# Optimization experiments

Measured on AMD Instinct MI355X. Metric: run time of the kernel, lower is better.

Reference implementation:

```python
import jax, jax.numpy as jnp
import numpy as np

V0 = 32000  # medicine vocab; SOS = V0, END = V0 + 1
E = 1024    # emb_dim


def setup_inputs() -> dict:
    key = jax.random.key(0)
    ks = jax.random.split(key, 12)
    s = 0.02
    return {
        "input_diagnosis": jax.random.randint(ks[0], (128,), 0, 35501),
        "input_procedure": jax.random.randint(ks[1], (64,), 0, 35501),
        "input_medicine": jax.random.randint(ks[2], (128,), 0, 35501),
        "dec_tokens": jax.random.randint(ks[3], (64,), 0, V0),
        "enc_emb": jax.random.normal(ks[4], (35501, E), jnp.float32) * s,
        "dec_emb": jax.random.normal(ks[5], (V0 + 2, E), jnp.float32) * s,
        "attn_w": jax.random.normal(ks[6], (1, 2 * E), jnp.float32) * s,
        "attn_b": jnp.zeros((1,), jnp.float32),
        "gru_w_ih": jax.random.normal(ks[7], (3 * E, 2 * E), jnp.float32) * s,
        "gru_w_hh": jax.random.normal(ks[8], (3 * E, E), jnp.float32) * s,
        "gru_b_ih": jnp.zeros((3 * E,), jnp.float32),
        "gru_b_hh": jnp.zeros((3 * E,), jnp.float32),
        "out_w": jax.random.normal(ks[9], (V0 + 2, E), jnp.float32) * s,
        "out_b": jnp.zeros((V0 + 2,), jnp.float32),
    }


def reference(input_diagnosis, input_procedure, input_medicine, dec_tokens,
              enc_emb, dec_emb, attn_w, attn_b,
              gru_w_ih, gru_w_hh, gru_b_ih, gru_b_hh, out_w, out_b):
    # Context: concat of the three code-set embeddings -> [L, E]
    ctx = jnp.concatenate([enc_emb[input_diagnosis],
                           enc_emb[input_procedure],
                           enc_emb[input_medicine]], axis=0)
    # Teacher-forced decoder token sequence: [SOS] + targets -> [T]
    tokens = jnp.concatenate([jnp.array([V0], dec_tokens.dtype), dec_tokens])
    dec_x = dec_emb[tokens]  # [T, E]
    h0 = dec_x[0]            # hidden init = SOS embedding (hidden_state None branch)
    # Additive attention Linear(2E,1): split weight into hidden part / context part
    w_h = attn_w[0, :E]
    w_e = attn_w[0, E:]
    ctx_score = ctx @ w_e + attn_b[0]  # [L], precomputed once

    def step(h, x):
        scores = ctx_score + jnp.dot(h, w_h)          # [L]
        a = jax.nn.softmax(scores)
        c = a @ ctx                                    # [E] weighted context
        u = jnp.concatenate([c, x])                    # [2E] GRU input
        gi = gru_w_ih @ u + gru_b_ih
        gh = gru_w_hh @ h + gru_b_hh
        ir, iz, in_ = jnp.split(gi, 3)
        hr, hz, hn = jnp.split(gh, 3)
        r = jax.nn.sigmoid(ir + hr)
        z = jax.nn.sigmoid(iz + hz)
        n = jnp.tanh(in_ + r * hn)
        h_new = (1.0 - z) * n + z * h                  # PyTorch GRU cell
        logits = out_w @ jax.nn.relu(h_new) + out_b    # [V0+2]
        return h_new, logits

    _, logits = jax.lax.scan(step, h0, dec_x)          # [T, V0+2]
    return logits
```

## Files before the change

kernel.cpp:

```cpp
#include <hip/hip_runtime.h>
#include <hip/hip_cooperative_groups.h>

typedef unsigned long long u64;
#define V0TOK 32000
#define EDIM  1024

__device__ __forceinline__ float dot4(float4 a, float4 b) {
    return fmaf(a.x, b.x, fmaf(a.y, b.y, fmaf(a.z, b.z, a.w * b.w)));
}

__global__ __launch_bounds__(512, 1) void k_rnn(
    const int* __restrict__ diag, const int* __restrict__ proc,
    const int* __restrict__ med,  const int* __restrict__ dtok,
    const float* __restrict__ enc, const float* __restrict__ dec,
    const float* __restrict__ attw,
    const float* __restrict__ wih, const float* __restrict__ whh,
    const float* __restrict__ bih, const float* __restrict__ bhh,
    float* __restrict__ ctx_ws, float* __restrict__ c_ws,
    unsigned* __restrict__ cnt, float* __restrict__ hbuf,
    float* __restrict__ hrelu)
{
    const int b = blockIdx.x, tid = threadIdx.x;
    const int w = tid >> 6, l = tid & 63;

    __shared__ float Wx[24 * 1024];
    __shared__ float sm[320];
    __shared__ float red1[8], red2[8];
    __shared__ float hlds[1024];

    if (tid == 0)
        __hip_atomic_store(&cnt[b * 16], 0u, __ATOMIC_RELAXED, __HIP_MEMORY_SCOPE_AGENT);
    if (b < 40) {
        int i = 8*b + w;
        int ridx = (i < 128) ? diag[i] : (i < 192 ? proc[i-128] : med[i-192]);
        const float4* row = (const float4*)(enc + (size_t)ridx * EDIM);
        const float4* we  = (const float4*)(attw + EDIM);
        float p = 0.f;
        #pragma unroll
        for (int m = 0; m < 4; m++) p += dot4(row[l + 64*m], we[l + 64*m]);
        #pragma unroll
        for (int off = 32; off; off >>= 1) p += __shfl_xor(p, off);
        if (l == 0) ctx_ws[i] = p;
    }
    __threadfence();
    cooperative_groups::this_grid().sync();
    __threadfence();

    {
        float s1 = (tid < 320) ? ctx_ws[tid] : -1e30f;
        float mx = s1;
        #pragma unroll
        for (int off = 32; off; off >>= 1) mx = fmaxf(mx, __shfl_xor(mx, off));
        if (l == 0) red1[w] = mx;
        __syncthreads();
        mx = red1[0];
        #pragma unroll
        for (int k = 1; k < 8; k++) mx = fmaxf(mx, red1[k]);
        float e1 = (tid < 320) ? expf(s1 - mx) : 0.f;
        float ss = e1;
        #pragma unroll
        for (int off = 32; off; off >>= 1) ss += __shfl_xor(ss, off);
        if (l == 0) red2[w] = ss;
        __syncthreads();
        float tot = red2[0];
        #pragma unroll
        for (int k = 1; k < 8; k++) tot += red2[k];
        if (tid < 320) sm[tid] = e1 / tot;
        __syncthreads();

        int e = 8*b + w;
        float p = 0.f;
        for (int i = l; i < 320; i += 64) {
            int ridx = (i < 128) ? diag[i] : (i < 192 ? proc[i-128] : med[i-192]);
            p += sm[i] * enc[(size_t)ridx * EDIM + e];
        }
        #pragma unroll
        for (int off = 32; off; off >>= 1) p += __shfl_xor(p, off);
        if (l == 0) c_ws[e] = p;
    }
    __threadfence();
    cooperative_groups::this_grid().sync();
    __threadfence();

    const int jr = 8*b + w, jz = 1024 + jr, jn = 2048 + jr;

    {
        const float4* s_r = (const float4*)(wih + (size_t)jr * 2048 + 1024);
        const float4* s_z = (const float4*)(wih + (size_t)jz * 2048 + 1024);
        const float4* s_n = (const float4*)(wih + (size_t)jn * 2048 + 1024);
        float4* d_r = (float4*)(Wx + (0*8 + w) * 1024);
        float4* d_z = (float4*)(Wx + (1*8 + w) * 1024);
        float4* d_n = (float4*)(Wx + (2*8 + w) * 1024);
        #pragma unroll
        for (int m = 0; m < 4; m++) {
            d_r[l + 64*m] = s_r[l + 64*m];
            d_z[l + 64*m] = s_z[l + 64*m];
            d_n[l + 64*m] = s_n[l + 64*m];
        }
    }

    float4 whr[4], whz[4], whn[4];
    {
        const float4* qr = (const float4*)(whh + (size_t)jr * 1024);
        const float4* qz = (const float4*)(whh + (size_t)jz * 1024);
        const float4* qn = (const float4*)(whh + (size_t)jn * 1024);
        #pragma unroll
        for (int m = 0; m < 4; m++) { whr[m] = qr[l + 64*m]; whz[m] = qz[l + 64*m]; whn[m] = qn[l + 64*m]; }
    }

    float4 c4[4], h4[4];
    {
        const float4* cp = (const float4*)c_ws;
        const float4* hp = (const float4*)(dec + (size_t)V0TOK * EDIM);
        #pragma unroll
        for (int m = 0; m < 4; m++) { c4[m] = cp[l + 64*m]; h4[m] = hp[l + 64*m]; }
    }
    const float b_r  = bih[jr] + bhh[jr];
    const float b_z  = bih[jz] + bhh[jz];
    const float b_ni = bih[jn];
    const float b_nh = bhh[jn];

    float gic_r = 0.f, gic_z = 0.f, gic_n = 0.f;
    {
        const float4* pr = (const float4*)(wih + (size_t)jr * 2048);
        const float4* pz = (const float4*)(wih + (size_t)jz * 2048);
        const float4* pn = (const float4*)(wih + (size_t)jn * 2048);
        #pragma unroll
        for (int m = 0; m < 4; m++) {
            gic_r += dot4(pr[l + 64*m], c4[m]);
            gic_z += dot4(pz[l + 64*m], c4[m]);
            gic_n += dot4(pn[l + 64*m], c4[m]);
        }
    }

    __syncthreads();

    const float4* WxR = (const float4*)(Wx + (0*8 + w) * 1024);
    const float4* WxZ = (const float4*)(Wx + (1*8 + w) * 1024);
    const float4* WxN = (const float4*)(Wx + (2*8 + w) * 1024);

    int tokreg = dtok[l];

    float gxr = gic_r, gxz = gic_z, gxn = gic_n;
    #pragma unroll
    for (int m = 0; m < 4; m++) {
        gxr += dot4(WxR[l + 64*m], h4[m]);
        gxz += dot4(WxZ[l + 64*m], h4[m]);
        gxn += dot4(WxN[l + 64*m], h4[m]);
    }
    float4 xv[4];
    {
        int tok1 = __shfl(tokreg, 0);
        const float4* xp = (const float4*)(dec + (size_t)tok1 * EDIM);
        #pragma unroll
        for (int m = 0; m < 4; m++) xv[m] = xp[l + 64*m];
    }

    const int jmi = jr >> 8, jli = (jr & 255) >> 2, jci = jr & 3;

    for (int t = 0; t < 65; t++) {
        float hr = 0.f, hz = 0.f, hn_ = 0.f;
        #pragma unroll
        for (int m = 0; m < 4; m++) {
            hr  += dot4(whr[m], h4[m]);
            hz  += dot4(whz[m], h4[m]);
            hn_ += dot4(whn[m], h4[m]);
        }
        float sr = gxr + hr, sz = gxz + hz, sni = gxn, snh = hn_;
        #pragma unroll
        for (int off = 32; off; off >>= 1) {
            sr  += __shfl_xor(sr, off);  sz  += __shfl_xor(sz, off);
            sni += __shfl_xor(sni, off); snh += __shfl_xor(snh, off);
        }
        float rg = 1.f / (1.f + expf(-(sr + b_r)));
        float zg = 1.f / (1.f + expf(-(sz + b_z)));
        float ng = tanhf(sni + b_ni + rg * (snh + b_nh));

        float4 hs = (jmi == 0) ? h4[0] : (jmi == 1) ? h4[1] : (jmi == 2) ? h4[2] : h4[3];
        float hv0 = (jci == 0) ? hs.x : (jci == 1) ? hs.y : (jci == 2) ? hs.z : hs.w;
        float hv = __shfl(hv0, jli);
        float hnew = (1.f - zg) * ng + zg * hv;

        if (t < 64) {
            const int par = (t + 1) & 1;
            if (l == 0) {
                hrelu[t * 1024 + jr] = fmaxf(hnew, 0.f);
                __hip_atomic_store(&hbuf[par * 1024 + jr], hnew,
                                   __ATOMIC_RELAXED, __HIP_MEMORY_SCOPE_AGENT);
            }
            __syncthreads();
            if (tid == 0)
                __hip_atomic_fetch_add(&cnt[b * 16], 1u,
                                       __ATOMIC_RELAXED, __HIP_MEMORY_SCOPE_AGENT);

            gxr = gic_r; gxz = gic_z; gxn = gic_n;
            #pragma unroll
            for (int m = 0; m < 4; m++) {
                gxr += dot4(WxR[l + 64*m], xv[m]);
                gxz += dot4(WxZ[l + 64*m], xv[m]);
                gxn += dot4(WxN[l + 64*m], xv[m]);
            }
            if (t < 63) {
                int tok = __shfl(tokreg, t + 1);
                const float4* xp = (const float4*)(dec + (size_t)tok * EDIM);
                #pragma unroll
                for (int m = 0; m < 4; m++) xv[m] = xp[l + 64*m];
            }

            if (tid < 128) {
                const unsigned target = (unsigned)(t + 1);
                while (__hip_atomic_load(&cnt[tid * 16], __ATOMIC_RELAXED,
                                         __HIP_MEMORY_SCOPE_AGENT) < target)
                    __builtin_amdgcn_s_sleep(1);
            }
            __syncthreads();

            u64 v = __hip_atomic_load((u64*)hbuf + par * 512 + tid,
                                      __ATOMIC_RELAXED, __HIP_MEMORY_SCOPE_AGENT);
            ((u64*)hlds)[tid] = v;
            __syncthreads();
            #pragma unroll
            for (int m = 0; m < 4; m++) h4[m] = ((const float4*)hlds)[l + 64*m];
        } else {
            if (l == 0) hrelu[64 * 1024 + jr] = fmaxf(hnew, 0.f);
        }
    }
}

__global__ __launch_bounds__(512) void k_logits(
    const float* __restrict__ wo, const float* __restrict__ bo,
    const float* __restrict__ hrelu, float* __restrict__ out)
{
    __shared__ float Hs[65 * 68];
    const int tid = threadIdx.x;
    const int q = tid & 15, s = (tid >> 4) & 7, g = tid >> 7;
    const int v0 = blockIdx.x * 32;
    const int vb = v0 + 8 * g;

    const float* wbase = wo + (size_t)((vb < 32002) ? vb : 0) * 1024;

    float acc[8][9];
    #pragma unroll
    for (int r = 0; r < 8; r++)
        #pragma unroll
        for (int ti = 0; ti < 9; ti++) acc[r][ti] = 0.f;

    for (int kc = 0; kc < 16; kc++) {
        __syncthreads();
        for (int idx = tid; idx < 65 * 16; idx += 512) {
            int t = idx >> 4, m = idx & 15;
            *(float4*)(Hs + t * 68 + 4 * m) =
                *(const float4*)(hrelu + t * 1024 + kc * 64 + 4 * m);
        }
        float4 wv[8];
        #pragma unroll
        for (int r = 0; r < 8; r++) {
            int v = vb + r;
            const float* wr = (v < 32002) ? (wbase + (size_t)r * 1024) : wbase;
            wv[r] = *(const float4*)(wr + kc * 64 + 4 * q);
        }
        __syncthreads();

        #pragma unroll
        for (int ti = 0; ti < 9; ti++) {
            int t = s + 8 * ti;
            if (t < 65) {
                float4 h4 = *(const float4*)(Hs + t * 68 + 4 * q);
                #pragma unroll
                for (int r = 0; r < 8; r++) {
                    acc[r][ti] = fmaf(wv[r].x, h4.x, acc[r][ti]);
                    acc[r][ti] = fmaf(wv[r].y, h4.y, acc[r][ti]);
                    acc[r][ti] = fmaf(wv[r].z, h4.z, acc[r][ti]);
                    acc[r][ti] = fmaf(wv[r].w, h4.w, acc[r][ti]);
                }
            }
        }
    }

    __syncthreads();
    float* Os = Hs;
    #pragma unroll
    for (int ti = 0; ti < 9; ti++) {
        int t = s + 8 * ti;
        #pragma unroll
        for (int r = 0; r < 8; r++) {
            float sum = acc[r][ti];
            sum += __shfl_xor(sum, 1);
            sum += __shfl_xor(sum, 2);
            sum += __shfl_xor(sum, 4);
            sum += __shfl_xor(sum, 8);
            if (q == 0 && t < 65) Os[t * 33 + 8 * g + r] = sum;
        }
    }
    __syncthreads();
    for (int idx = tid; idx < 65 * 32; idx += 512) {
        int t = idx >> 5, c = idx & 31;
        int v = v0 + c;
        if (v < 32002) out[(size_t)t * 32002 + v] = Os[t * 33 + c] + bo[v];
    }
}

extern "C" void kernel_launch(void* const* d_in, const int* in_sizes, int n_in,
                              void* d_out, int out_size, void* d_ws, size_t ws_size,
                              hipStream_t stream) {
    const int*   diag = (const int*)d_in[0];
    const int*   proc = (const int*)d_in[1];
    const int*   med  = (const int*)d_in[2];
    const int*   dtok = (const int*)d_in[3];
    const float* enc  = (const float*)d_in[4];
    const float* dec  = (const float*)d_in[5];
    const float* attw = (const float*)d_in[6];
    const float* wih  = (const float*)d_in[8];
    const float* whh  = (const float*)d_in[9];
    const float* bih  = (const float*)d_in[10];
    const float* bhh  = (const float*)d_in[11];
    const float* wo   = (const float*)d_in[12];
    const float* bo   = (const float*)d_in[13];
    float* out = (float*)d_out;

    float*    ctx_ws = (float*)d_ws;
    float*    c_ws   = (float*)((char*)d_ws + 2048);
    unsigned* cnt    = (unsigned*)((char*)d_ws + 8192);
    float*    hbuf   = (float*)((char*)d_ws + 16384);
    float*    hrelu  = (float*)((char*)d_ws + 32768);

    void* args[] = { (void*)&diag, (void*)&proc, (void*)&med, (void*)&dtok,
                     (void*)&enc, (void*)&dec, (void*)&attw,
                     (void*)&wih, (void*)&whh, (void*)&bih, (void*)&bhh,
                     (void*)&ctx_ws, (void*)&c_ws, (void*)&cnt, (void*)&hbuf,
                     (void*)&hrelu };
    hipLaunchCooperativeKernel((void*)k_rnn, dim3(128), dim3(512), args, 0, stream);

    k_logits<<<dim3(1001), dim3(512), 0, stream>>>(wo, bo, hrelu, out);
}
```

Measured before the change: 512.7 us.

## Replace counter barrier with tagged hidden-state polling and retile logits GEMV

The recurrent kernel drops the per-block arrival counters and their syncthreads-plus-atomic barrier. Each block now writes its hidden values packed with a step tag into 64-bit slots, and readers spin until every slot carries the current tag. This removes a round trip through the counters and lets each element be consumed as soon as it arrives, but every thread now spins on global memory. Separately, the logits kernel is retiled to 16 vocab rows per 256-thread block with 65 accumulators per thread and a software-prefetched hrelu/weight stage, trading register pressure for lower LDS traffic and better occupancy.

```diff
diff --git a/kernel.cpp b/kernel.cpp
--- a/kernel.cpp
+++ b/kernel.cpp
@@ -17,8 +17,7 @@
     const float* __restrict__ wih, const float* __restrict__ whh,
     const float* __restrict__ bih, const float* __restrict__ bhh,
     float* __restrict__ ctx_ws, float* __restrict__ c_ws,
-    unsigned* __restrict__ cnt, float* __restrict__ hbuf,
-    float* __restrict__ hrelu)
+    u64* __restrict__ hbuf, float* __restrict__ hrelu)
 {
     const int b = blockIdx.x, tid = threadIdx.x;
     const int w = tid >> 6, l = tid & 63;
@@ -28,8 +27,9 @@
     __shared__ float red1[8], red2[8];
     __shared__ float hlds[1024];
 
-    if (tid == 0)
-        __hip_atomic_store(&cnt[b * 16], 0u, __ATOMIC_RELAXED, __HIP_MEMORY_SCOPE_AGENT);
+    if (b < 4)
+        __hip_atomic_store(&hbuf[b * 512 + tid], 0ull,
+                           __ATOMIC_RELAXED, __HIP_MEMORY_SCOPE_AGENT);
     if (b < 40) {
         int i = 8*b + w;
         int ridx = (i < 128) ? diag[i] : (i < 192 ? proc[i-128] : med[i-192]);
@@ -156,7 +156,7 @@
         for (int m = 0; m < 4; m++) xv[m] = xp[l + 64*m];
     }
 
-    const int jmi = jr >> 8, jli = (jr & 255) >> 2, jci = jr & 3;
+    const int jmi = jr >> 8, jli = (jr >> 2) & 63, jci = jr & 3;
 
     for (int t = 0; t < 65; t++) {
         float hr = 0.f, hz = 0.f, hn_ = 0.f;
@@ -183,15 +183,13 @@
 
         if (t < 64) {
             const int par = (t + 1) & 1;
+            const unsigned tag = (unsigned)(t + 1);
             if (l == 0) {
                 hrelu[t * 1024 + jr] = fmaxf(hnew, 0.f);
-                __hip_atomic_store(&hbuf[par * 1024 + jr], hnew,
+                u64 pk = ((u64)tag << 32) | (u64)__float_as_uint(hnew);
+                __hip_atomic_store(&hbuf[par * 1024 + jr], pk,
                                    __ATOMIC_RELAXED, __HIP_MEMORY_SCOPE_AGENT);
             }
-            __syncthreads();
-            if (tid == 0)
-                __hip_atomic_fetch_add(&cnt[b * 16], 1u,
-                                       __ATOMIC_RELAXED, __HIP_MEMORY_SCOPE_AGENT);
 
             gxr = gic_r; gxz = gic_z; gxn = gic_n;
             #pragma unroll
@@ -207,96 +205,98 @@
                 for (int m = 0; m < 4; m++) xv[m] = xp[l + 64*m];
             }
 
-            if (tid < 128) {
-                const unsigned target = (unsigned)(t + 1);
-                while (__hip_atomic_load(&cnt[tid * 16], __ATOMIC_RELAXED,
-                                         __HIP_MEMORY_SCOPE_AGENT) < target)
-                    __builtin_amdgcn_s_sleep(1);
+            {
+                u64* hb = hbuf + par * 1024;
+                u64 va, vb2;
+                while (1) {
+                    va  = __hip_atomic_load(&hb[2*tid],     __ATOMIC_RELAXED, __HIP_MEMORY_SCOPE_AGENT);
+                    vb2 = __hip_atomic_load(&hb[2*tid + 1], __ATOMIC_RELAXED, __HIP_MEMORY_SCOPE_AGENT);
+                    if (((unsigned)(va >> 32) == tag) & ((unsigned)(vb2 >> 32) == tag)) break;
+                }
+                hlds[2*tid]     = __uint_as_float((unsigned)va);
+                hlds[2*tid + 1] = __uint_as_float((unsigned)vb2);
             }
-            __syncthreads();
-
-            u64 v = __hip_atomic_load((u64*)hbuf + par * 512 + tid,
-                                      __ATOMIC_RELAXED, __HIP_MEMORY_SCOPE_AGENT);
-            ((u64*)hlds)[tid] = v;
             __syncthreads();
             #pragma unroll
             for (int m = 0; m < 4; m++) h4[m] = ((const float4*)hlds)[l + 64*m];
+            __syncthreads();
         } else {
             if (l == 0) hrelu[64 * 1024 + jr] = fmaxf(hnew, 0.f);
         }
     }
 }
 
-__global__ __launch_bounds__(512) void k_logits(
+__global__ __launch_bounds__(256, 4) void k_logits(
     const float* __restrict__ wo, const float* __restrict__ bo,
     const float* __restrict__ hrelu, float* __restrict__ out)
 {
     __shared__ float Hs[65 * 68];
-    const int tid = threadIdx.x;
-    const int q = tid & 15, s = (tid >> 4) & 7, g = tid >> 7;
-    const int v0 = blockIdx.x * 32;
-    const int vb = v0 + 8 * g;
-
-    const float* wbase = wo + (size_t)((vb < 32002) ? vb : 0) * 1024;
-
-    float acc[8][9];
+    const int tid = threadIdx.x, q = tid & 15, vl = tid >> 4;
+    const int v0 = blockIdx.x * 16;
+    const int v  = v0 + vl;
+    const int vc = (v < 32002) ? v : 32001;
+    const float* wrow = wo + (size_t)vc * 1024;
+
+    float acc[65];
     #pragma unroll
-    for (int r = 0; r < 8; r++)
-        #pragma unroll
-        for (int ti = 0; ti < 9; ti++) acc[r][ti] = 0.f;
+    for (int t = 0; t < 65; t++) acc[t] = 0.f;
+
+    float4 st0, st1, st2, st3, st4;
+    #define ISSUE(kc_) do {                                                   \
+        int base = (kc_) * 64;                                                \
+        { int idx = tid;       st0 = *(const float4*)(hrelu + (idx>>4)*1024 + base + 4*(idx&15)); } \
+        { int idx = tid + 256; st1 = *(const float4*)(hrelu + (idx>>4)*1024 + base + 4*(idx&15)); } \
+        { int idx = tid + 512; st2 = *(const float4*)(hrelu + (idx>>4)*1024 + base + 4*(idx&15)); } \
+        { int idx = tid + 768; st3 = *(const float4*)(hrelu + (idx>>4)*1024 + base + 4*(idx&15)); } \
+        if (tid < 16) st4 = *(const float4*)(hrelu + 64*1024 + base + 4*tid); \
+    } while (0)
+    #define WRITE() do {                                                      \
+        { int idx = tid;       *(float4*)(Hs + (idx>>4)*68 + 4*(idx&15)) = st0; } \
+        { int idx = tid + 256; *(float4*)(Hs + (idx>>4)*68 + 4*(idx&15)) = st1; } \
+        { int idx = tid + 512; *(float4*)(Hs + (idx>>4)*68 + 4*(idx&15)) = st2; } \
+        { int idx = tid + 768; *(float4*)(Hs + (idx>>4)*68 + 4*(idx&15)) = st3; } \
+        if (tid < 16) *(float4*)(Hs + 64*68 + 4*tid) = st4;                   \
+    } while (0)
+
+    ISSUE(0);
+    float4 wv = *(const float4*)(wrow + 4*q);
 
     for (int kc = 0; kc < 16; kc++) {
-        __syncthreads();
-        for (int idx = tid; idx < 65 * 16; idx += 512) {
-            int t = idx >> 4, m = idx & 15;
-            *(float4*)(Hs + t * 68 + 4 * m) =
-                *(const float4*)(hrelu + t * 1024 + kc * 64 + 4 * m);
-        }
-        float4 wv[8];
-        #pragma unroll
-        for (int r = 0; r < 8; r++) {
-            int v = vb + r;
-            const float* wr = (v < 32002) ? (wbase + (size_t)r * 1024) : wbase;
-            wv[r] = *(const float4*)(wr + kc * 64 + 4 * q);
-        }
-        __syncthreads();
-
-        #pragma unroll
-        for (int ti = 0; ti < 9; ti++) {
-            int t = s + 8 * ti;
-            if (t < 65) {
-                float4 h4 = *(const float4*)(Hs + t * 68 + 4 * q);
-                #pragma unroll
-                for (int r = 0; r < 8; r++) {
-                    acc[r][ti] = fmaf(wv[r].x, h4.x, acc[r][ti]);
-                    acc[r][ti] = fmaf(wv[r].y, h4.y, acc[r][ti]);
-                    acc[r][ti] = fmaf(wv[r].z, h4.z, acc[r][ti]);
-                    acc[r][ti] = fmaf(wv[r].w, h4.w, acc[r][ti]);
-                }
-            }
-        }
-    }
-
-    __syncthreads();
+        WRITE();
+        __syncthreads();
+        float4 wnext;
+        if (kc < 15) {
+            ISSUE(kc + 1);
+            wnext = *(const float4*)(wrow + (kc + 1) * 64 + 4*q);
+        }
+        const float* hp = Hs + 4*q;
+        #pragma unroll
+        for (int t = 0; t < 65; t++) {
+            float4 h4 = *(const float4*)(hp + t * 68);
+            acc[t] = fmaf(wv.x, h4.x, acc[t]);
+            acc[t] = fmaf(wv.y, h4.y, acc[t]);
+            acc[t] = fmaf(wv.z, h4.z, acc[t]);
+            acc[t] = fmaf(wv.w, h4.w, acc[t]);
+        }
+        wv = wnext;
+        __syncthreads();
+    }
+
     float* Os = Hs;
     #pragma unroll
-    for (int ti = 0; ti < 9; ti++) {
-        int t = s + 8 * ti;
-        #pragma unroll
-        for (int r = 0; r < 8; r++) {
-            float sum = acc[r][ti];
-            sum += __shfl_xor(sum, 1);
-            sum += __shfl_xor(sum, 2);
-            sum += __shfl_xor(sum, 4);
-            sum += __shfl_xor(sum, 8);
-            if (q == 0 && t < 65) Os[t * 33 + 8 * g + r] = sum;
-        }
+    for (int t = 0; t < 65; t++) {
+        float s_ = acc[t];
+        s_ += __shfl_xor(s_, 1);
+        s_ += __shfl_xor(s_, 2);
+        s_ += __shfl_xor(s_, 4);
+        s_ += __shfl_xor(s_, 8);
+        if (q == 0) Os[t * 17 + vl] = s_;
     }
     __syncthreads();
-    for (int idx = tid; idx < 65 * 32; idx += 512) {
-        int t = idx >> 5, c = idx & 31;
-        int v = v0 + c;
-        if (v < 32002) out[(size_t)t * 32002 + v] = Os[t * 33 + c] + bo[v];
+    for (int idx = tid; idx < 65 * 16; idx += 256) {
+        int t = idx >> 4, c = idx & 15;
+        int vv = v0 + c;
+        if (vv < 32002) out[(size_t)t * 32002 + vv] = Os[t * 17 + c] + bo[vv];
     }
 }
 
@@ -318,18 +318,16 @@
     const float* bo   = (const float*)d_in[13];
     float* out = (float*)d_out;
 
-    float*    ctx_ws = (float*)d_ws;
-    float*    c_ws   = (float*)((char*)d_ws + 2048);
-    unsigned* cnt    = (unsigned*)((char*)d_ws + 8192);
-    float*    hbuf   = (float*)((char*)d_ws + 16384);
-    float*    hrelu  = (float*)((char*)d_ws + 32768);
+    float* ctx_ws = (float*)d_ws;
+    float* c_ws   = (float*)((char*)d_ws + 2048);
+    u64*   hbuf   = (u64*)  ((char*)d_ws + 16384);
+    float* hrelu  = (float*)((char*)d_ws + 32768);
 
     void* args[] = { (void*)&diag, (void*)&proc, (void*)&med, (void*)&dtok,
                      (void*)&enc, (void*)&dec, (void*)&attw,
                      (void*)&wih, (void*)&whh, (void*)&bih, (void*)&bhh,
-                     (void*)&ctx_ws, (void*)&c_ws, (void*)&cnt, (void*)&hbuf,
-                     (void*)&hrelu };
+                     (void*)&ctx_ws, (void*)&c_ws, (void*)&hbuf, (void*)&hrelu };
     hipLaunchCooperativeKernel((void*)k_rnn, dim3(128), dim3(512), args, 0, stream);
 
-    k_logits<<<dim3(1001), dim3(512), 0, stream>>>(wo, bo, hrelu, out);
+    k_logits<<<dim3(2001), dim3(256), 0, stream>>>(wo, bo, hrelu, out);
 }
```

New measurement: 461.5 us. 10.0% less time.
